# Kernel tuning notes

Hardware: AMD Instinct MI355X
Metric: run time of the kernel (lower is better)

## Reference

```python
import jax, jax.numpy as jnp
import numpy as np


def _tconv(x, w, b):
    # x: [B,C_in,N,T], w: [C_out,C_in,1,k] -> 'same' padding along T only
    pad = (w.shape[-1] - 1) // 2
    y = jax.lax.conv_general_dilated(x, w, (1, 1), [(0, 0), (pad, pad)],
                                     dimension_numbers=('NCHW', 'OIHW', 'NCHW'))
    return y + b[None, :, None, None]


def _temporal(x, w1, b1, w2, b2, w3, b3):
    # x: [B,T,N,C] -> gated GLU-style temporal conv -> [B,T,N,C_out]
    xc = jnp.transpose(x, (0, 3, 2, 1))  # [B,C,N,T]
    p = _tconv(xc, w1, b1)
    q = jax.nn.sigmoid(_tconv(xc, w2, b2))
    h = jax.nn.relu(p * q + _tconv(xc, w3, b3))
    return jnp.transpose(h, (0, 3, 2, 1))


def _cheb(x, src, dst, wn, W, bias):
    # x: [M,N,C]; scaled Laplacian with lambda_max=2 => L_hat = -D^-1/2 A D^-1/2
    # (diag +1 from L and -1 self-loop fill cancel exactly, as in PyG ChebConv)
    N = x.shape[1]

    def spmv(v):
        msgs = v[:, src, :] * wn[None, :, None]
        return jnp.zeros_like(v).at[:, dst, :].add(msgs)

    Tx0 = x
    out = jnp.einsum('mnc,cd->mnd', Tx0, W[0])
    Tx1 = spmv(Tx0)
    out = out + jnp.einsum('mnc,cd->mnd', Tx1, W[1])
    Txp, Txpp = Tx1, Tx0
    for k in range(2, W.shape[0]):
        Txk = 2.0 * spmv(Txp) - Txpp
        out = out + jnp.einsum('mnc,cd->mnd', Txk, W[k])
        Txpp, Txp = Txp, Txk
    return out + bias


def _bn_train(out, gamma, beta, eps=1e-5):
    # BatchNorm2d in training mode (batch stats, biased variance) over [B,C,N,T]
    ob = jnp.transpose(out, (0, 3, 2, 1))
    mu = jnp.mean(ob, axis=(0, 2, 3), keepdims=True)
    var = jnp.mean((ob - mu) ** 2, axis=(0, 2, 3), keepdims=True)
    ob = (ob - mu) * jax.lax.rsqrt(var + eps)
    ob = ob * gamma[None, :, None, None] + beta[None, :, None, None]
    return jnp.transpose(ob, (0, 3, 2, 1))


def setup_inputs():
    B, T, N, Cin, H, k, K, E = 16, 12, 4096, 2, 64, 3, 3, 65536
    ks = jax.random.split(jax.random.key(0), 20)
    sc = 0.1
    return {
        'x': jax.random.normal(ks[0], (B, T, N, Cin), jnp.float32),
        'edge_index': jax.random.randint(ks[1], (2, E), 0, N),
        'edge_attr': jax.random.uniform(ks[2], (E,), jnp.float32),
        't1_w1': jax.random.normal(ks[3], (H, Cin, 1, k), jnp.float32) * sc,
        't1_b1': jnp.zeros((H,), jnp.float32),
        't1_w2': jax.random.normal(ks[4], (H, Cin, 1, k), jnp.float32) * sc,
        't1_b2': jnp.zeros((H,), jnp.float32),
        't1_w3': jax.random.normal(ks[5], (H, Cin, 1, k), jnp.float32) * sc,
        't1_b3': jnp.zeros((H,), jnp.float32),
        'cheb_W': jax.random.normal(ks[6], (K, H, H), jnp.float32) * sc,
        'cheb_b': jnp.zeros((H,), jnp.float32),
        't2_w1': jax.random.normal(ks[7], (H, H, 1, k), jnp.float32) * sc,
        't2_b1': jnp.zeros((H,), jnp.float32),
        't2_w2': jax.random.normal(ks[8], (H, H, 1, k), jnp.float32) * sc,
        't2_b2': jnp.zeros((H,), jnp.float32),
        't2_w3': jax.random.normal(ks[9], (H, H, 1, k), jnp.float32) * sc,
        't2_b3': jnp.zeros((H,), jnp.float32),
        'bn_g': jnp.ones((H,), jnp.float32),
        'bn_b': jnp.zeros((H,), jnp.float32),
    }


def reference(x, edge_index, edge_attr,
              t1_w1, t1_b1, t1_w2, t1_b2, t1_w3, t1_b3,
              cheb_W, cheb_b,
              t2_w1, t2_b1, t2_w2, t2_b2, t2_w3, t2_b3,
              bn_g, bn_b):
    t1 = _temporal(x, t1_w1, t1_b1, t1_w2, t1_b2, t1_w3, t1_b3)  # [B,T,N,H]
    B, T, N, C = t1.shape
    src, dst = edge_index[0], edge_index[1]
    # sym normalization: deg from source scatter; -D^-1/2 w D^-1/2 edge weights
    deg = jnp.zeros((N,), t1.dtype).at[src].add(edge_attr)
    safe = jnp.where(deg > 0, deg, 1.0)
    dis = jnp.where(deg > 0, jax.lax.rsqrt(safe), 0.0)
    wn = -dis[src] * edge_attr * dis[dst]
    g = _cheb(t1.reshape(B * T, N, C), src, dst, wn, cheb_W, cheb_b)
    g = jax.nn.relu(g).reshape(B, T, N, C)
    out = _temporal(g, t2_w1, t2_b1, t2_w2, t2_b2, t2_w3, t2_b3)
    return _bn_train(out, bn_g, bn_b)
```

## Files before the change

### kernel.cpp

```cpp
#include <hip/hip_runtime.h>
#include <stdint.h>

#define BB 16
#define TT 12
#define NN 4096
#define HH 64
#define EE 65536
#define MM (BB*TT)
#define ROWS (MM*NN)
#define TOT (ROWS*HH)
#define NBUCKET 256
#define T2_GRID 2048
#define T2_NT 6

typedef __attribute__((ext_vector_type(8))) __bf16 bf16x8;
typedef __attribute__((ext_vector_type(8))) unsigned short us8;
typedef __attribute__((ext_vector_type(4))) float f32x4;
typedef __attribute__((ext_vector_type(2))) unsigned int ui2;

__device__ __forceinline__ unsigned short f2bf(float f){
  unsigned u = __builtin_bit_cast(unsigned, f);
  u += 0x7fffu + ((u >> 16) & 1u);
  return (unsigned short)(u >> 16);
}
__device__ __forceinline__ float bf2f(unsigned short s){
  unsigned u = ((unsigned)s) << 16;
  return __builtin_bit_cast(float, u);
}
__device__ __forceinline__ float lo2f(unsigned v){ return __builtin_bit_cast(float, v << 16); }
__device__ __forceinline__ float hi2f(unsigned v){ return __builtin_bit_cast(float, v & 0xffff0000u); }
__device__ __forceinline__ bf16x8 ldbf8(const unsigned short* p){
  us8 u = *reinterpret_cast<const us8*>(p);
  return __builtin_bit_cast(bf16x8, u);
}


__global__ void k_deg_cnt(const int* __restrict__ src, const int* __restrict__ dst,
                          const float* __restrict__ attr,
                          float* __restrict__ deg, int* __restrict__ cnt){
  int e = blockIdx.x * 256 + threadIdx.x;
  if (e < EE){
    atomicAdd(&deg[src[e]], attr[e]);
    atomicAdd(&cnt[dst[e]], 1);
  }
}

__global__ void k_wn(const int* __restrict__ src, const int* __restrict__ dst,
                     const float* __restrict__ attr, const float* __restrict__ deg,
                     float* __restrict__ wn){
  int e = blockIdx.x * 256 + threadIdx.x;
  if (e < EE){
    float ds = deg[src[e]], dd = deg[dst[e]];
    float rs = ds > 0.f ? rsqrtf(ds) : 0.f;
    float rd = dd > 0.f ? rsqrtf(dd) : 0.f;
    wn[e] = -rs * attr[e] * rd;
  }
}

__global__ void k_scan(const int* __restrict__ cnt, int* __restrict__ rowptr,
                       int* __restrict__ fill){
  __shared__ int lds[1024];
  int t = threadIdx.x;
  int c0 = cnt[4*t], c1 = cnt[4*t+1], c2 = cnt[4*t+2], c3 = cnt[4*t+3];
  int s = c0 + c1 + c2 + c3;
  lds[t] = s; __syncthreads();
  for (int off = 1; off < 1024; off <<= 1){
    int v = (t >= off) ? lds[t-off] : 0;
    __syncthreads();
    lds[t] += v;
    __syncthreads();
  }
  int excl = lds[t] - s;
  rowptr[4*t]   = excl;            fill[4*t]   = excl;
  rowptr[4*t+1] = excl + c0;       fill[4*t+1] = excl + c0;
  rowptr[4*t+2] = excl + c0 + c1;  fill[4*t+2] = excl + c0 + c1;
  rowptr[4*t+3] = excl + c0+c1+c2; fill[4*t+3] = excl + c0+c1+c2;
  if (t == 1023) rowptr[4096] = lds[1023];
}

__global__ void k_csr(const int* __restrict__ dst, const int* __restrict__ src,
                      const float* __restrict__ wn, int* __restrict__ fill,
                      ui2* __restrict__ csre){
  int e = blockIdx.x * 256 + threadIdx.x;
  if (e < EE){
    int d = dst[e];
    int pos = atomicAdd(&fill[d], 1);
    ui2 mw;
    mw.x = (unsigned)src[e];
    mw.y = __builtin_bit_cast(unsigned, wn[e]);
    csre[pos] = mw;
  }
}


__global__ void k_wprep(const float* __restrict__ chebW,
                        const float* __restrict__ w1, const float* __restrict__ w2,
                        const float* __restrict__ w3,
                        const float* __restrict__ e1w, const float* __restrict__ e1b,
                        const float* __restrict__ e2w, const float* __restrict__ e2b,
                        const float* __restrict__ e3w, const float* __restrict__ e3b,
                        unsigned short* __restrict__ wfD, unsigned short* __restrict__ wfF,
                        unsigned short* __restrict__ wfE){
  int gt = blockIdx.x * blockDim.x + threadIdx.x;
  int stride = gridDim.x * blockDim.x;
  for (int i = gt; i < 12288; i += stride){
    int kl = i & 31, cc = (i >> 5) & 63, mk = i >> 11;
    int kt = mk & 1, mat = mk >> 1;
    int k = kt * 32 + kl;
    float v;
    if (mat == 0)      v = chebW[k*64 + cc] - chebW[2*4096 + k*64 + cc];
    else if (mat == 1) v = chebW[4096 + k*64 + cc];
    else               v = 2.f * chebW[2*4096 + k*64 + cc];
    wfD[i] = f2bf(v);
  }
  for (int i = gt; i < 36864; i += stride){
    int kl = i & 31, hh = (i >> 5) & 63, ck = i >> 11;
    int kt = ck % 6, conv = ck / 6;
    int k = kt * 32 + kl, dt = k >> 6, ci = k & 63;
    const float* w = (conv == 0) ? w1 : ((conv == 1) ? w2 : w3);
    wfF[i] = f2bf(w[(hh*64 + ci)*3 + dt]);
  }
  for (int i = gt; i < 6144; i += stride){
    int k = i & 31, hh = (i >> 5) & 63, conv = i >> 11;
    const float* w = (conv == 0) ? e1w : ((conv == 1) ? e2w : e3w);
    const float* b = (conv == 0) ? e1b : ((conv == 1) ? e2b : e3b);
    float v = 0.f;
    if (k < 6)       v = w[(hh*2 + (k & 1))*3 + (k >> 1)];
    else if (k == 6) v = b[hh];
    wfE[i] = f2bf(v);
  }
}


__global__ __launch_bounds__(256) void k_temporal1(
    const float* __restrict__ x, const unsigned short* __restrict__ wfE,
    unsigned short* __restrict__ U){
  const int tid = threadIdx.x;
  const int wv = tid >> 6, lane = tid & 63;
  const int lhi = lane >> 4, llo = lane & 15;
  const int blk = blockIdx.x;
  const int bt = blk >> 6, nb = blk & 63;
  const int t = bt - (bt / TT) * TT;

  us8 au = {0,0,0,0,0,0,0,0};
  if (lhi == 0){
    const int n = nb*64 + wv*16 + llo;
    #pragma unroll
    for (int dt = 0; dt < 3; ++dt){
      int tp = t + dt - 1;
      if (tp >= 0 && tp < TT){
        const float2 v = *reinterpret_cast<const float2*>(
            x + ((size_t)(bt + dt - 1) * NN + n) * 2);
        if (dt == 0){ au[0] = f2bf(v.x); au[1] = f2bf(v.y); }
        if (dt == 1){ au[2] = f2bf(v.x); au[3] = f2bf(v.y); }
        if (dt == 2){ au[4] = f2bf(v.x); au[5] = f2bf(v.y); }
      }
    }
    au[6] = 0x3f80;
  }
  const bf16x8 af = __builtin_bit_cast(bf16x8, au);

  const f32x4 z = {0.f, 0.f, 0.f, 0.f};
  f32x4 acc[3][4];
  #pragma unroll
  for (int conv = 0; conv < 3; ++conv)
    #pragma unroll
    for (int ht = 0; ht < 4; ++ht){
      bf16x8 bw = ldbf8(wfE + (size_t)((conv*64) + ht*16 + llo)*32 + lhi*8);
      acc[conv][ht] = __builtin_amdgcn_mfma_f32_16x16x32_bf16(af, bw, z, 0, 0, 0);
    }

  #pragma unroll
  for (int ht = 0; ht < 4; ++ht){
    const int h = ht*16 + llo;
    #pragma unroll
    for (int i = 0; i < 4; ++i){
      float p = acc[0][ht][i];
      float q = acc[1][ht][i];
      float r = acc[2][ht][i];
      float sig = 1.f / (1.f + __expf(-q));
      float o = fmaxf(fmaf(p, sig, r), 0.f);
      const int n = nb*64 + wv*16 + lhi*4 + i;
      U[((size_t)n * MM + bt) * 64 + h] = f2bf(o);
    }
  }
}


__global__ __launch_bounds__(256) void k_fused_sc(
    const unsigned short* __restrict__ U,
    const int* __restrict__ rowptr, const ui2* __restrict__ csre,
    const unsigned short* __restrict__ wfD, const float* __restrict__ cheb_b,
    unsigned short* __restrict__ G0bf, unsigned short* __restrict__ P){
  __shared__ unsigned short vlds[4096];
  const int tid = threadIdx.x;
  int blk = blockIdx.x;
  blk = (blk & 7) * (12288 >> 3) + (blk >> 3);
  const int n = blk / 3, mb = blk - n*3;

  const int e0 = __builtin_amdgcn_readfirstlane(rowptr[n]);
  const int e1 = __builtin_amdgcn_readfirstlane(rowptr[n+1]);
  const unsigned short* Ubt = U + mb*4096 + tid*4;

  f32x4 acc[4];
  #pragma unroll
  for (int k = 0; k < 4; ++k) acc[k] = {0.f, 0.f, 0.f, 0.f};

  for (int e = e0; e < e1; e += 4){
    int ss[4]; float ww[4];
    #pragma unroll
    for (int u = 0; u < 4; ++u){
      const int ee = e + u;
      const bool in = ee < e1;
      const ui2 mw = csre[in ? ee : e0];
      ss[u] = (int)__builtin_amdgcn_readfirstlane(mw.x);
      const float wv = __builtin_bit_cast(float, __builtin_amdgcn_readfirstlane(mw.y));
      ww[u] = in ? wv : 0.f;
    }
    ui2 d[4][4];
    #pragma unroll
    for (int u = 0; u < 4; ++u){
      const unsigned short* rp = Ubt + (size_t)ss[u] * 12288;
      #pragma unroll
      for (int k = 0; k < 4; ++k)
        d[u][k] = *reinterpret_cast<const ui2*>(rp + k*1024);
    }
    #pragma unroll
    for (int u = 0; u < 4; ++u){
      const float w = ww[u];
      #pragma unroll
      for (int k = 0; k < 4; ++k){
        acc[k][0] = fmaf(w, lo2f(d[u][k].x), acc[k][0]);
        acc[k][1] = fmaf(w, hi2f(d[u][k].x), acc[k][1]);
        acc[k][2] = fmaf(w, lo2f(d[u][k].y), acc[k][2]);
        acc[k][3] = fmaf(w, hi2f(d[u][k].y), acc[k][3]);
      }
    }
  }

  #pragma unroll
  for (int k = 0; k < 4; ++k){
    const int q = tid + k*256;
    const int m = q >> 4, c4 = q & 15;
    const int byteoff = m*128 + ((c4*8) ^ ((m & 7) << 4));
    ushort4 pk;
    pk.x = f2bf(acc[k][0]); pk.y = f2bf(acc[k][1]);
    pk.z = f2bf(acc[k][2]); pk.w = f2bf(acc[k][3]);
    *reinterpret_cast<ushort4*>(reinterpret_cast<char*>(vlds) + byteoff) = pk;
  }
  __syncthreads();

  const int wv = tid >> 6, lane = tid & 63;
  const int lhi = lane >> 4, llo = lane & 15;
  const int c = wv * 16 + llo;
  const size_t growbase = (size_t)blk * 64;

  bf16x8 bA[2], bW1[2], bW2[2];
  #pragma unroll
  for (int kt = 0; kt < 2; ++kt){
    bA[kt]  = ldbf8(wfD + (size_t)((0*2 + kt)*64 + c)*32 + lhi*8);
    bW1[kt] = ldbf8(wfD + (size_t)((1*2 + kt)*64 + c)*32 + lhi*8);
    bW2[kt] = ldbf8(wfD + (size_t)((2*2 + kt)*64 + c)*32 + lhi*8);
  }
  const f32x4 z = {0.f, 0.f, 0.f, 0.f};
  f32x4 accG[4], accP[4];
  #pragma unroll
  for (int rt = 0; rt < 4; ++rt){ accG[rt] = z; accP[rt] = z; }

  #pragma unroll
  for (int rt = 0; rt < 4; ++rt){
    const int m = rt*16 + llo;
    const unsigned short* up = U + (growbase + m)*64 + lhi*8;
    #pragma unroll
    for (int kt = 0; kt < 2; ++kt){
      bf16x8 au = ldbf8(up + kt*32);
      const int vboff = m*128 + (((kt*64) + lhi*16) ^ ((m & 7) << 4));
      bf16x8 av = __builtin_bit_cast(bf16x8, *reinterpret_cast<const us8*>(
          reinterpret_cast<const char*>(vlds) + vboff));
      accG[rt] = __builtin_amdgcn_mfma_f32_16x16x32_bf16(au, bA[kt],  accG[rt], 0, 0, 0);
      accG[rt] = __builtin_amdgcn_mfma_f32_16x16x32_bf16(av, bW1[kt], accG[rt], 0, 0, 0);
      accP[rt] = __builtin_amdgcn_mfma_f32_16x16x32_bf16(av, bW2[kt], accP[rt], 0, 0, 0);
    }
  }
  const float bias = cheb_b[c];
  #pragma unroll
  for (int rt = 0; rt < 4; ++rt){
    #pragma unroll
    for (int i = 0; i < 4; ++i){
      const size_t row = growbase + rt*16 + lhi*4 + i;
      G0bf[row*64 + c] = f2bf(accG[rt][i] + bias);
      P[row*64 + c]    = f2bf(accP[rt][i]);
    }
  }
}


__global__ __launch_bounds__(256) void k_spmv2(
    const unsigned short* __restrict__ X,
    const int* __restrict__ rowptr,
    const ui2* __restrict__ csre,
    const unsigned short* __restrict__ G0bf,
    unsigned short* __restrict__ Y){
  constexpr int EU = 16;
  const int nb = gridDim.x;
  int bs = (blockIdx.x & 7) * (nb >> 3) + (blockIdx.x >> 3);
  int wg = bs * 4 + (threadIdx.x >> 6);
  wg = __builtin_amdgcn_readfirstlane(wg);
  const int lane = threadIdx.x & 63;
  const int mg = wg >> 12, n = wg & (NN-1);
  const int e0 = __builtin_amdgcn_readfirstlane(rowptr[n]);
  const int e1 = __builtin_amdgcn_readfirstlane(rowptr[n+1]);
  const unsigned short* Xmg = X + (size_t)mg * 256;
  const int loff = lane * 4;

  float a0 = 0.f, a1 = 0.f, a2 = 0.f, a3 = 0.f;

  for (int e = e0; e < e1; e += EU){
    int ss[EU]; float ww[EU];
    #pragma unroll
    for (int u = 0; u < EU; ++u){
      const int ee = e + u;
      const bool in = ee < e1;
      const ui2 mw = csre[in ? ee : e0];
      ss[u] = (int)__builtin_amdgcn_readfirstlane(mw.x);
      const float wv = __builtin_bit_cast(float, __builtin_amdgcn_readfirstlane(mw.y));
      ww[u] = in ? wv : 0.f;
    }
    ui2 d[EU];
    #pragma unroll
    for (int u = 0; u < EU; ++u)
      d[u] = *reinterpret_cast<const ui2*>(Xmg + (size_t)ss[u] * 12288 + loff);
    #pragma unroll
    for (int u = 0; u < EU; ++u){
      const float w = ww[u];
      a0 = fmaf(w, lo2f(d[u].x), a0);
      a1 = fmaf(w, hi2f(d[u].x), a1);
      a2 = fmaf(w, lo2f(d[u].y), a2);
      a3 = fmaf(w, hi2f(d[u].y), a3);
    }
  }

  const size_t oidx = (size_t)n * 12288 + mg * 256 + loff;
  {
    ui2 gd = *reinterpret_cast<const ui2*>(G0bf + oidx);
    a0 = fmaxf(a0 + lo2f(gd.x), 0.f);
    a1 = fmaxf(a1 + hi2f(gd.x), 0.f);
    a2 = fmaxf(a2 + lo2f(gd.y), 0.f);
    a3 = fmaxf(a3 + hi2f(gd.y), 0.f);
  }
  ui2 o;
  o.x = (unsigned)f2bf(a0) | ((unsigned)f2bf(a1) << 16);
  o.y = (unsigned)f2bf(a2) | ((unsigned)f2bf(a3) << 16);
  *reinterpret_cast<ui2*>(Y + oidx) = o;
}


__device__ __forceinline__ void t2_load(const unsigned short* __restrict__ g,
                                        int tile, int tid, uint4* st){
  const int bt = tile >> 6, nb = tile & 63;
  const int t = bt - (bt / TT) * TT;
  #pragma unroll
  for (int j = 0; j < 6; ++j){
    const int plane = j >> 1;
    const int tp = t + plane - 1;
    const int idx = ((j & 1) << 8) + tid;
    const int row = idx >> 3;
    const int innerb = (idx & 7) * 16;
    if (tp >= 0 && tp < TT){
      const unsigned short* sp = g
          + ((size_t)(nb*64 + row) * MM + (bt + plane - 1)) * 64
          + ((innerb ^ ((row & 7) << 4)) >> 1);
      st[j] = *reinterpret_cast<const uint4*>(sp);
    } else {
      st[j] = make_uint4(0u, 0u, 0u, 0u);
    }
  }
}

__global__ __launch_bounds__(256, 2) void k_temporal2(
    const unsigned short* __restrict__ g,
    const unsigned short* __restrict__ wfF,
    const float* __restrict__ b1, const float* __restrict__ b2, const float* __restrict__ b3,
    unsigned short* __restrict__ obf, float* __restrict__ bnstat2){
  __shared__ unsigned short smem[2][12288];
  const int tid = threadIdx.x;
  const int wv = tid >> 6, lane = tid & 63;
  const int lhi = lane >> 4, llo = lane & 15;
  const int h = wv * 16 + llo;
  const int h0 = wv * 16 + lhi * 4;

  bf16x8 bw[3][6];
  #pragma unroll
  for (int cv = 0; cv < 3; ++cv)
    #pragma unroll
    for (int kt = 0; kt < 6; ++kt)
      bw[cv][kt] = ldbf8(wfF + (size_t)((cv*6 + kt)*64 + h)*32 + lhi*8);

  const f32x4 vb1 = *reinterpret_cast<const f32x4*>(b1 + h0);
  const f32x4 vb2 = *reinterpret_cast<const f32x4*>(b2 + h0);
  const f32x4 vb3 = *reinterpret_cast<const f32x4*>(b3 + h0);
  const f32x4 z = {0.f, 0.f, 0.f, 0.f};

  uint4 st[6];
  t2_load(g, blockIdx.x, tid, st);
  #pragma unroll
  for (int j = 0; j < 6; ++j)
    *reinterpret_cast<uint4*>(&smem[0][(size_t)(j*256 + tid) * 8]) = st[j];
  __syncthreads();

  int cur = 0;
  for (int it = 0; it < T2_NT; ++it){
    const int tile = blockIdx.x + it * T2_GRID;
    const int bt = tile >> 6, nb = tile & 63;

    if (it + 1 < T2_NT)
      t2_load(g, tile + T2_GRID, tid, st);

    const unsigned short* sb = smem[cur];
    f32x4 acc[3][4];
    #pragma unroll
    for (int cv = 0; cv < 3; ++cv)
      #pragma unroll
      for (int rt = 0; rt < 4; ++rt) acc[cv][rt] = z;

    #pragma unroll
    for (int kt = 0; kt < 6; ++kt){
      const int dt = kt >> 1;
      const int qb = (kt & 1) * 64 + lhi * 16;
      #pragma unroll
      for (int rt = 0; rt < 4; ++rt){
        const int row = rt*16 + llo;
        bf16x8 a = __builtin_bit_cast(bf16x8, *reinterpret_cast<const us8*>(
            sb + dt*4096 + row*64 + ((qb ^ ((row & 7) << 4)) >> 1)));
        acc[0][rt] = __builtin_amdgcn_mfma_f32_16x16x32_bf16(bw[0][kt], a, acc[0][rt], 0, 0, 0);
        acc[1][rt] = __builtin_amdgcn_mfma_f32_16x16x32_bf16(bw[1][kt], a, acc[1][rt], 0, 0, 0);
        acc[2][rt] = __builtin_amdgcn_mfma_f32_16x16x32_bf16(bw[2][kt], a, acc[2][rt], 0, 0, 0);
      }
    }

    f32x4 lsum = z, lsq = z;
    #pragma unroll
    for (int rt = 0; rt < 4; ++rt){
      const int n = nb*64 + rt*16 + llo;
      ushort4 pk;
      unsigned short* pp = reinterpret_cast<unsigned short*>(&pk);
      #pragma unroll
      for (int i = 0; i < 4; ++i){
        float p = acc[0][rt][i] + vb1[i];
        float q = acc[1][rt][i] + vb2[i];
        float r = acc[2][rt][i] + vb3[i];
        float sig = 1.f / (1.f + __expf(-q));
        float o = fmaxf(fmaf(p, sig, r), 0.f);
        pp[i] = f2bf(o);
        lsum[i] += o; lsq[i] = fmaf(o, o, lsq[i]);
      }
      *reinterpret_cast<ushort4*>(&obf[((size_t)bt * NN + n) * 64 + h0]) = pk;
    }
    #pragma unroll
    for (int m = 1; m < 16; m <<= 1){
      #pragma unroll
      for (int i = 0; i < 4; ++i){
        lsum[i] += __shfl_xor(lsum[i], m);
        lsq[i]  += __shfl_xor(lsq[i], m);
      }
    }
    if (llo == 0){
      float* bs = bnstat2 + (size_t)(tile & (NBUCKET-1)) * 128;
      #pragma unroll
      for (int i = 0; i < 4; ++i){
        atomicAdd(&bs[h0 + i], lsum[i]);
        atomicAdd(&bs[64 + h0 + i], lsq[i]);
      }
    }

    if (it + 1 < T2_NT){
      #pragma unroll
      for (int j = 0; j < 6; ++j)
        *reinterpret_cast<uint4*>(&smem[cur ^ 1][(size_t)(j*256 + tid) * 8]) = st[j];
      __syncthreads();
      cur ^= 1;
    }
  }
}


__global__ void k_bnfinal(const float* __restrict__ bnstat2, float* __restrict__ bnstat){
  int t = threadIdx.x;
  float s = 0.f;
  for (int b = 0; b < NBUCKET; ++b) s += bnstat2[(size_t)b * 128 + t];
  bnstat[t] = s;
}

__global__ __launch_bounds__(256) void k_bnapply(
    const unsigned short* __restrict__ obf, float* __restrict__ out,
    const float* __restrict__ bnstat,
    const float* __restrict__ gamma, const float* __restrict__ beta){
  __shared__ float ssc[64], sfb[64];
  int tid = threadIdx.x;
  if (tid < 64){
    const float inv = 1.f / (float)ROWS;
    float s = bnstat[tid], q = bnstat[64 + tid];
    float mu = s * inv;
    float var = q * inv - mu * mu;
    if (var < 0.f) var = 0.f;
    float sc = gamma[tid] * rsqrtf(var + 1e-5f);
    ssc[tid] = sc;
    sfb[tid] = beta[tid] - mu * sc;
  }
  __syncthreads();
  const int ngrp = TOT / 8;
  for (int i = blockIdx.x * 256 + tid; i < ngrp; i += gridDim.x * 256){
    us8 v = *reinterpret_cast<const us8*>(obf + (size_t)i * 8);
    const int c0 = (i * 8) & 63;
    f32x4 lo, hi;
    #pragma unroll
    for (int j = 0; j < 4; ++j)
      lo[j] = fmaf(bf2f(v[j]), ssc[c0 + j], sfb[c0 + j]);
    #pragma unroll
    for (int j = 0; j < 4; ++j)
      hi[j] = fmaf(bf2f(v[4 + j]), ssc[c0 + 4 + j], sfb[c0 + 4 + j]);
    *reinterpret_cast<f32x4*>(out + (size_t)i * 8)     = lo;
    *reinterpret_cast<f32x4*>(out + (size_t)i * 8 + 4) = hi;
  }
}


extern "C" void kernel_launch(void* const* d_in, const int* in_sizes, int n_in,
                              void* d_out, int out_size, void* d_ws, size_t ws_size,
                              hipStream_t stream){
  const float* x     = (const float*)d_in[0];
  const int*   ei    = (const int*)d_in[1];
  const float* attr  = (const float*)d_in[2];
  const float* t1w1  = (const float*)d_in[3];
  const float* t1b1  = (const float*)d_in[4];
  const float* t1w2  = (const float*)d_in[5];
  const float* t1b2  = (const float*)d_in[6];
  const float* t1w3  = (const float*)d_in[7];
  const float* t1b3  = (const float*)d_in[8];
  const float* chebW = (const float*)d_in[9];
  const float* chebB = (const float*)d_in[10];
  const float* t2w1  = (const float*)d_in[11];
  const float* t2b1  = (const float*)d_in[12];
  const float* t2w2  = (const float*)d_in[13];
  const float* t2b2  = (const float*)d_in[14];
  const float* t2w3  = (const float*)d_in[15];
  const float* t2b3  = (const float*)d_in[16];
  const float* bng   = (const float*)d_in[17];
  const float* bnb   = (const float*)d_in[18];
  const int* src = ei;
  const int* dst = ei + EE;

  const size_t SZ_U = (size_t)ROWS * 64 * 2;
  char* ws = (char*)d_ws;
  unsigned short* bufA = (unsigned short*)ws;
  unsigned short* bufB = (unsigned short*)(ws + SZ_U);
  size_t off = 2 * SZ_U;
  float* deg    = (float*)(ws + off); off += 4096 * 4;
  int*   cnt    = (int*)(ws + off);   off += 4096 * 4;
  int*   rowptr = (int*)(ws + off);   off += 4128 * 4;
  int*   fill   = (int*)(ws + off);   off += 4096 * 4;
  float* wn     = (float*)(ws + off); off += EE * 4;
  ui2*   csre   = (ui2*)(ws + off);   off += EE * 8;
  unsigned short* wfD = (unsigned short*)(ws + off); off += 12288 * 2;
  unsigned short* wfF = (unsigned short*)(ws + off); off += 36864 * 2;
  unsigned short* wfE = (unsigned short*)(ws + off); off += 6144 * 2;
  float* bnstat = (float*)(ws + off); off += 128 * 4;
  float* bnstat2 = (float*)(ws + off); off += NBUCKET * 128 * 4;

  unsigned short* G0bf = (unsigned short*)d_out;

  hipMemsetAsync(deg, 0, 4096 * 4, stream);
  hipMemsetAsync(cnt, 0, 4096 * 4, stream);
  hipMemsetAsync(bnstat2, 0, NBUCKET * 128 * 4, stream);

  k_deg_cnt<<<EE/256, 256, 0, stream>>>(src, dst, attr, deg, cnt);
  k_wn<<<EE/256, 256, 0, stream>>>(src, dst, attr, deg, wn);
  k_scan<<<1, 1024, 0, stream>>>(cnt, rowptr, fill);
  k_csr<<<EE/256, 256, 0, stream>>>(dst, src, wn, fill, csre);
  k_wprep<<<64, 256, 0, stream>>>(chebW, t2w1, t2w2, t2w3,
                                  t1w1, t1b1, t1w2, t1b2, t1w3, t1b3,
                                  wfD, wfF, wfE);

  k_temporal1<<<ROWS/64, 256, 0, stream>>>(x, wfE, bufA );
  k_fused_sc<<<ROWS/64, 256, 0, stream>>>(bufA , rowptr, csre, wfD, chebB,
                                          G0bf, bufB );
  k_spmv2<<<(MM/4)*NN/4, 256, 0, stream>>>(bufB , rowptr, csre, G0bf, bufA );
  k_temporal2<<<T2_GRID, 256, 0, stream>>>(bufA , wfF, t2b1, t2b2, t2b3,
                                           bufB , bnstat2);
  k_bnfinal<<<1, 128, 0, stream>>>(bnstat2, bnstat);
  k_bnapply<<<2048, 256, 0, stream>>>(bufB , (float*)d_out, bnstat, bng, bnb);
}
```

Before: 682.8 us.

## Retile fused Chebyshev SpMV block to 16 nodes by 4 time rows

Each block previously gathered neighbours for one node across a third of the 192 batch-time rows. It now handles 16 nodes by 4 batch-time rows, with each wave walking the edge lists of 4 nodes unrolled by 8 edges. Every gathered neighbour row is a contiguous 512-byte chunk rather than four strided pieces, so the number of edge-list loads per row changes. The MFMA stage and the output writes are re-indexed to the new row mapping. In exchange, each edge is now read by 48 blocks instead of 3, and per-node degree imbalance now serializes within a wave.

```diff
diff --git a/kernel.cpp b/kernel.cpp
--- a/kernel.cpp
+++ b/kernel.cpp
@@ -195,65 +195,55 @@
   __shared__ unsigned short vlds[4096];
   const int tid = threadIdx.x;
   int blk = blockIdx.x;
-  blk = (blk & 7) * (12288 >> 3) + (blk >> 3);
-  const int n = blk / 3, mb = blk - n*3;
-
-  const int e0 = __builtin_amdgcn_readfirstlane(rowptr[n]);
-  const int e1 = __builtin_amdgcn_readfirstlane(rowptr[n+1]);
-  const unsigned short* Ubt = U + mb*4096 + tid*4;
-
-  f32x4 acc[4];
-  #pragma unroll
-  for (int k = 0; k < 4; ++k) acc[k] = {0.f, 0.f, 0.f, 0.f};
-
-  for (int e = e0; e < e1; e += 4){
-    int ss[4]; float ww[4];
-    #pragma unroll
-    for (int u = 0; u < 4; ++u){
-      const int ee = e + u;
-      const bool in = ee < e1;
-      const ui2 mw = csre[in ? ee : e0];
-      ss[u] = (int)__builtin_amdgcn_readfirstlane(mw.x);
-      const float wv = __builtin_bit_cast(float, __builtin_amdgcn_readfirstlane(mw.y));
-      ww[u] = in ? wv : 0.f;
-    }
-    ui2 d[4][4];
-    #pragma unroll
-    for (int u = 0; u < 4; ++u){
-      const unsigned short* rp = Ubt + (size_t)ss[u] * 12288;
-      #pragma unroll
-      for (int k = 0; k < 4; ++k)
-        d[u][k] = *reinterpret_cast<const ui2*>(rp + k*1024);
-    }
-    #pragma unroll
-    for (int u = 0; u < 4; ++u){
-      const float w = ww[u];
-      #pragma unroll
-      for (int k = 0; k < 4; ++k){
-        acc[k][0] = fmaf(w, lo2f(d[u][k].x), acc[k][0]);
-        acc[k][1] = fmaf(w, hi2f(d[u][k].x), acc[k][1]);
-        acc[k][2] = fmaf(w, lo2f(d[u][k].y), acc[k][2]);
-        acc[k][3] = fmaf(w, hi2f(d[u][k].y), acc[k][3]);
-      }
-    }
-  }
-
-  #pragma unroll
-  for (int k = 0; k < 4; ++k){
-    const int q = tid + k*256;
-    const int m = q >> 4, c4 = q & 15;
-    const int byteoff = m*128 + ((c4*8) ^ ((m & 7) << 4));
+  blk = (blk & 7) * 1536 + (blk >> 3);
+  const int mg = blk >> 8;
+  const int ng = blk & 255;
+  const int wv = tid >> 6, lane = tid & 63;
+  const int p = lane >> 4, c4 = lane & 15;
+  const int loff = p*64 + c4*4;
+
+  const unsigned short* Umg = U + (size_t)mg * 256;
+
+  #pragma unroll
+  for (int j = 0; j < 4; ++j){
+    const int n = ng*16 + wv*4 + j;
+    const int e0 = __builtin_amdgcn_readfirstlane(rowptr[n]);
+    const int e1 = __builtin_amdgcn_readfirstlane(rowptr[n+1]);
+    float a0 = 0.f, a1 = 0.f, a2 = 0.f, a3 = 0.f;
+    for (int e = e0; e < e1; e += 8){
+      int ss[8]; float ww[8];
+      #pragma unroll
+      for (int u = 0; u < 8; ++u){
+        const int ee = e + u;
+        const bool in = ee < e1;
+        const ui2 mw = csre[in ? ee : e0];
+        ss[u] = (int)__builtin_amdgcn_readfirstlane(mw.x);
+        const float wvv = __builtin_bit_cast(float, __builtin_amdgcn_readfirstlane(mw.y));
+        ww[u] = in ? wvv : 0.f;
+      }
+      ui2 d[8];
+      #pragma unroll
+      for (int u = 0; u < 8; ++u)
+        d[u] = *reinterpret_cast<const ui2*>(Umg + (size_t)ss[u] * 12288 + loff);
+      #pragma unroll
+      for (int u = 0; u < 8; ++u){
+        const float w = ww[u];
+        a0 = fmaf(w, lo2f(d[u].x), a0);
+        a1 = fmaf(w, hi2f(d[u].x), a1);
+        a2 = fmaf(w, lo2f(d[u].y), a2);
+        a3 = fmaf(w, hi2f(d[u].y), a3);
+      }
+    }
+    const int r = (wv*4 + j)*4 + p;
+    const int byteoff = r*128 + ((c4*8) ^ ((r & 7) << 4));
     ushort4 pk;
-    pk.x = f2bf(acc[k][0]); pk.y = f2bf(acc[k][1]);
-    pk.z = f2bf(acc[k][2]); pk.w = f2bf(acc[k][3]);
+    pk.x = f2bf(a0); pk.y = f2bf(a1); pk.z = f2bf(a2); pk.w = f2bf(a3);
     *reinterpret_cast<ushort4*>(reinterpret_cast<char*>(vlds) + byteoff) = pk;
   }
   __syncthreads();
 
-  const int wv = tid >> 6, lane = tid & 63;
   const int lhi = lane >> 4, llo = lane & 15;
   const int c = wv * 16 + llo;
-  const size_t growbase = (size_t)blk * 64;
 
   bf16x8 bA[2], bW1[2], bW2[2];
   #pragma unroll
@@ -270,7 +260,8 @@
   #pragma unroll
   for (int rt = 0; rt < 4; ++rt){
     const int m = rt*16 + llo;
-    const unsigned short* up = U + (growbase + m)*64 + lhi*8;
+    const size_t gr = ((size_t)(ng*16 + (m >> 2))) * MM + mg*4 + (m & 3);
+    const unsigned short* up = U + gr*64 + lhi*8;
     #pragma unroll
     for (int kt = 0; kt < 2; ++kt){
       bf16x8 au = ldbf8(up + kt*32);
@@ -287,9 +278,10 @@
   for (int rt = 0; rt < 4; ++rt){
     #pragma unroll
     for (int i = 0; i < 4; ++i){
-      const size_t row = growbase + rt*16 + lhi*4 + i;
-      G0bf[row*64 + c] = f2bf(accG[rt][i] + bias);
-      P[row*64 + c]    = f2bf(accP[rt][i]);
+      const int mrow = rt*16 + lhi*4 + i;
+      const size_t gr = ((size_t)(ng*16 + (mrow >> 2))) * MM + mg*4 + (mrow & 3);
+      G0bf[gr*64 + c] = f2bf(accG[rt][i] + bias);
+      P[gr*64 + c]    = f2bf(accP[rt][i]);
     }
   }
 }
```

Result: faster. 640.1 us (median of 2 runs) (-6.2%).
